# Kernel optimization log

Measured on AMD Instinct MI355X. Metric: run time of the kernel, lower is better.

The kernel has to match this reference:

```python
import jax, jax.numpy as jnp
import numpy as np

H = 16        # num query heads
HKV = 1       # num key/value heads (MQA; source matmul broadcasts only for 1 or H)
D = 128       # head_dim
SCALE = 1.0 / np.sqrt(D)


def setup_inputs() -> dict:
    key = jax.random.key(0)
    k1, k2, k3 = jax.random.split(key, 3)
    B, S, HID = 2, 2048, 2048
    hidden_states = jax.random.normal(k1, (B, S, HID), dtype=jnp.float32)
    # real RoPE tables: cos/sin of shape [S, D]
    inv_freq = 1.0 / (10000.0 ** (np.arange(0, D, 2, dtype=np.float32) / D))
    t = np.arange(S, dtype=np.float32)
    freqs = np.outer(t, inv_freq)                      # [S, D/2]
    emb = np.concatenate([freqs, freqs], axis=-1)      # [S, D]
    cos = jnp.asarray(np.cos(emb), dtype=jnp.float32)
    sin = jnp.asarray(np.sin(emb), dtype=jnp.float32)
    w_qkv = jax.random.normal(k2, (HID, (H + 2 * HKV) * D), dtype=jnp.float32) * (HID ** -0.5)
    w_o = jax.random.normal(k3, (H * D, HID), dtype=jnp.float32) * ((H * D) ** -0.5)
    return {"hidden_states": hidden_states, "cos": cos, "sin": sin,
            "w_qkv": w_qkv, "w_o": w_o}


def _rotate_half(x):
    x1, x2 = jnp.split(x, 2, axis=-1)
    return jnp.concatenate([-x2, x1], axis=-1)


def reference(hidden_states, cos, sin, w_qkv, w_o):
    B, S, _ = hidden_states.shape
    qkv = hidden_states @ w_qkv                        # [B,S,(H+2*HKV)*D]
    qkv = qkv.reshape(B, S, H + 2 * HKV, D)
    q = qkv[:, :, :H]                                  # [B,S,H,D]
    k = qkv[:, :, H:H + HKV]                           # [B,S,HKV,D]
    v = qkv[:, :, H + HKV:]                            # [B,S,HKV,D]
    c = cos[None, :, None, :]                          # [1,S,1,D]
    s = sin[None, :, None, :]
    q = q * c + _rotate_half(q) * s
    k = k * c + _rotate_half(k) * s
    # MQA: squeeze the single kv head
    k0 = k[:, :, 0]                                    # [B,S,D]
    v0 = v[:, :, 0]                                    # [B,S,D]
    qh = jnp.transpose(q, (0, 2, 1, 3))                # [B,H,S,D]
    scores = jnp.einsum('bhsd,btd->bhst', qh, k0) * SCALE
    attn = jax.nn.softmax(scores.astype(jnp.float32), axis=-1).astype(qh.dtype)
    out = jnp.einsum('bhst,btd->bhsd', attn, v0)       # [B,H,S,D]
    out = jnp.transpose(out, (0, 2, 1, 3)).reshape(B, S, H * D)
    return out @ w_o
```

## Files before the change

kernel.cpp:

```cpp
#include <hip/hip_runtime.h>

typedef __attribute__((ext_vector_type(8))) short bf16x8;
typedef __attribute__((ext_vector_type(4))) float f32x4;
typedef __attribute__((ext_vector_type(8))) unsigned short u16x8;
typedef __attribute__((ext_vector_type(2))) unsigned int u32x2;

#define H_Q   16
#define NH    18
#define SEQ   2048
#define BATCH 2
#define HID   2048
#define NQKV  2304
#define QK_SCALE2 0.1275174313f

__device__ __forceinline__ float bf2f(unsigned short u){
  union { unsigned int u; float f; } x; x.u = ((unsigned int)u) << 16; return x.f;
}
__device__ __forceinline__ unsigned short f2bf(float f){
  union { float f; unsigned int u; } x; x.f = f;
  unsigned int r = x.u + 0x7fffu + ((x.u >> 16) & 1u);
  return (unsigned short)(r >> 16);
}
__device__ __forceinline__ unsigned int cvtpk(float lo, float hi){
  unsigned int r;
  asm("v_cvt_pk_bf16_f32 %0, %1, %2" : "=v"(r) : "v"(lo), "v"(hi));
  return r;
}

__global__ __launch_bounds__(256) void convert_bf16(const float* __restrict__ src,
                                                    unsigned short* __restrict__ dst){
  const size_t i0 = ((size_t)blockIdx.x * 256 + threadIdx.x) * 16;
  f32x4 a = *(const f32x4*)(src + i0);
  f32x4 b = *(const f32x4*)(src + i0 + 4);
  f32x4 c = *(const f32x4*)(src + i0 + 8);
  f32x4 d = *(const f32x4*)(src + i0 + 12);
  u16x8 lo, hi;
#pragma unroll
  for (int j = 0; j < 4; ++j){
    lo[j] = f2bf(a[j]); lo[4+j] = f2bf(b[j]);
    hi[j] = f2bf(c[j]); hi[4+j] = f2bf(d[j]);
  }
  *(u16x8*)(dst + i0)     = lo;
  *(u16x8*)(dst + i0 + 8) = hi;
}

__global__ __launch_bounds__(256) void transpose_f2b(const float* __restrict__ W,
                                                     unsigned short* __restrict__ WT,
                                                     int K, int N){
  __shared__ float tile[64][72];
  const int t = threadIdx.x;
  const int nt = blockIdx.x * 64, kt = blockIdx.y * 64;
#pragma unroll
  for (int p = 0; p < 2; ++p){
    int slot = p*256 + t, r = slot >> 3, c = (slot & 7) * 8;
    *(f32x4*)&tile[r][c]     = *(const f32x4*)(W + (size_t)(kt + r)*N + nt + c);
    *(f32x4*)&tile[r][c + 4] = *(const f32x4*)(W + (size_t)(kt + r)*N + nt + c + 4);
  }
  __syncthreads();
#pragma unroll
  for (int p = 0; p < 2; ++p){
    int slot = p*256 + t, r = slot >> 3, c = (slot & 7) * 8;
    u16x8 v;
#pragma unroll
    for (int j = 0; j < 8; ++j) v[j] = f2bf(tile[c + j][r]);
    *(u16x8*)(WT + (size_t)(nt + r)*K + kt + c) = v;
  }
}

template<bool F32OUT>
__global__ __launch_bounds__(256, 2) void gemm_bt(const unsigned short* __restrict__ A,
                                                  const unsigned short* __restrict__ Bt,
                                                  void* __restrict__ Cv,
                                                  int M, int N, int K){
  __shared__ unsigned short lds[2][2][128*32];
  const int tid  = threadIdx.x;
  const int wave = tid >> 6, lane = tid & 63;
  const int row0 = blockIdx.x * 128, col0 = blockIdx.y * 128;
  const int wr = (wave >> 1) * 64, wc = (wave & 1) * 64;
  const int lm = lane & 15, lk = (lane >> 4) * 8;
  f32x4 acc[4][4] = {};

  auto stage = [&](int buf, int kt){
#pragma unroll
    for (int i = 0; i < 2; ++i){
      int slot = i*256 + tid;
      int r = slot >> 2, kc = (slot & 3) * 8;
      const unsigned short* ga = A  + (size_t)(row0 + r)*K + kt*32 + kc;
      const unsigned short* gb = Bt + (size_t)(col0 + r)*K + kt*32 + kc;
      unsigned short* la = &lds[buf][0][(i*256 + (wave << 6)) * 8];
      unsigned short* lb = &lds[buf][1][(i*256 + (wave << 6)) * 8];
      __builtin_amdgcn_global_load_lds((const __attribute__((address_space(1))) void*)ga,
                                       (__attribute__((address_space(3))) void*)la, 16, 0, 0);
      __builtin_amdgcn_global_load_lds((const __attribute__((address_space(1))) void*)gb,
                                       (__attribute__((address_space(3))) void*)lb, 16, 0, 0);
    }
  };

  stage(0, 0);
  const int KT = K >> 5;
  int buf = 0;
  for (int kt = 0; kt < KT; ++kt){
    __syncthreads();
    if (kt + 1 < KT) stage(buf ^ 1, kt + 1);
    const unsigned short* la = lds[buf][0];
    const unsigned short* lb = lds[buf][1];
    bf16x8 af[4], bfr[4];
#pragma unroll
    for (int i = 0; i < 4; ++i) af[i]  = *(const bf16x8*)&la[(wr + i*16 + lm)*32 + lk];
#pragma unroll
    for (int j = 0; j < 4; ++j) bfr[j] = *(const bf16x8*)&lb[(wc + j*16 + lm)*32 + lk];
#pragma unroll
    for (int i = 0; i < 4; ++i)
#pragma unroll
      for (int j = 0; j < 4; ++j)
        acc[i][j] = __builtin_amdgcn_mfma_f32_16x16x32_bf16(af[i], bfr[j], acc[i][j], 0, 0, 0);
    buf ^= 1;
  }

#pragma unroll
  for (int i = 0; i < 4; ++i){
    int row = row0 + wr + i*16 + (lane >> 4) * 4;
#pragma unroll
    for (int j = 0; j < 4; ++j){
      int col = col0 + wc + j*16 + lm;
#pragma unroll
      for (int r = 0; r < 4; ++r){
        if (F32OUT) ((float*)Cv)[(size_t)(row + r)*N + col] = acc[i][j][r];
        else ((unsigned short*)Cv)[(size_t)(row + r)*N + col] = f2bf(acc[i][j][r]);
      }
    }
  }
}

__global__ __launch_bounds__(256) void rope_pack(unsigned short* __restrict__ qkv,
                                                 const float* __restrict__ cosb,
                                                 const float* __restrict__ sinb,
                                                 unsigned short* __restrict__ Kb,
                                                 unsigned short* __restrict__ Vt){
  const int bs = blockIdx.x;
  const int s = bs & (SEQ-1), b = bs >> 11;
  const int t = threadIdx.x;
  unsigned short* row = qkv + (size_t)bs * NQKV;
  const float* cr = cosb + (size_t)s * 128;
  const float* sr = sinb + (size_t)s * 128;
  const int h = t >> 4, d0 = (t & 15) * 4;
  unsigned short* q = row + h * 128;
#pragma unroll
  for (int i = 0; i < 4; ++i){
    int d = d0 + i;
    float c  = cr[d], sn = sr[d];
    float x1 = bf2f(q[d]),  x2 = bf2f(q[d + 64]);
    q[d]      = f2bf((x1*c - x2*sn) * QK_SCALE2);
    q[d + 64] = f2bf((x2*c + x1*sn) * QK_SCALE2);
  }
  if (t < 64){
    const unsigned short* kk = row + H_Q*128;
    int d = t;
    float c  = cr[d], sn = sr[d];
    float x1 = bf2f(kk[d]), x2 = bf2f(kk[d + 64]);
    unsigned short* ko = Kb + ((size_t)b*SEQ + s)*128;
    ko[d]      = f2bf(x1*c - x2*sn);
    ko[d + 64] = f2bf(x2*c + x1*sn);
  }
  if (t < 128){
    Vt[((size_t)b*128 + t)*SEQ + s] = row[(H_Q + 1)*128 + t];
  }
}

__global__ __launch_bounds__(256, 2) void attn_fwd(const unsigned short* __restrict__ qkv,
                                                   const unsigned short* __restrict__ Kb,
                                                   const unsigned short* __restrict__ Vt,
                                                   unsigned short* __restrict__ Ob){
  __shared__ unsigned short kls[2][32*128];
  __shared__ unsigned short vls[2][128*32];
  const int tid = threadIdx.x, lane = tid & 63;
  const int g = lane >> 4, m = lane & 15;
  const int wg = blockIdx.x;
  const int bh = wg >> 4, qb = wg & 15;
  const int b = bh >> 4, h = bh & 15;
  const int q0 = qb * 128 + (tid >> 6) * 32;

  const unsigned short* qrowA = qkv + ((size_t)((b << 11) + q0 + m)*NH + h)*128;
  const unsigned short* qrowB = qrowA + (size_t)16*NH*128;
  bf16x8 qfA[4], qfB[4];
#pragma unroll
  for (int dc = 0; dc < 4; ++dc){
    qfA[dc] = *(const bf16x8*)(qrowA + dc*32 + g*8);
    qfB[dc] = *(const bf16x8*)(qrowB + dc*32 + g*8);
  }

  const unsigned short* Kbase = Kb + (size_t)b*SEQ*128;
  const unsigned short* Vbase = Vt + (size_t)b*128*SEQ;

  const int krow = tid >> 4;
  const int kchunk = (tid & 15) ^ (krow & 7);
  const int vrow = tid >> 2;
  const int vchunk = (tid & 3) ^ ((tid >> 3) & 3);

  auto stage = [&](int buf, int tile){
    const int n0 = tile * 32;
#pragma unroll
    for (int ck = 0; ck < 2; ++ck){
      const unsigned short* gp = Kbase + (size_t)(n0 + ck*16 + krow)*128 + kchunk*8;
      unsigned short* lp = &kls[buf][(ck*256 + tid) * 8];
      __builtin_amdgcn_global_load_lds((const __attribute__((address_space(1))) void*)gp,
                                       (__attribute__((address_space(3))) void*)lp, 16, 0, 0);
    }
#pragma unroll
    for (int cv = 0; cv < 2; ++cv){
      const unsigned short* gp = Vbase + (size_t)(cv*64 + vrow)*SEQ + n0 + vchunk*8;
      unsigned short* lp = &vls[buf][(cv*256 + tid) * 8];
      __builtin_amdgcn_global_load_lds((const __attribute__((address_space(1))) void*)gp,
                                       (__attribute__((address_space(3))) void*)lp, 16, 0, 0);
    }
  };

  f32x4 oA[8] = {}, oB[8] = {};
  float sA = 0.f, sB = 0.f;
  const int ksw = (m & 7);
  const int vsw = (m >> 1) & 3;

  stage(0, 0);
  stage(1, 1);
  const int NT = SEQ / 32;
  for (int t = 0; t < NT; ++t){
    const int cur = t & 1;
    if (t + 1 < NT) asm volatile("s_waitcnt vmcnt(4)" ::: "memory");
    else            asm volatile("s_waitcnt vmcnt(0)" ::: "memory");
    __builtin_amdgcn_s_barrier();

    const unsigned short* kb = kls[cur];
    const unsigned short* vb = vls[cur];

    bf16x8 kf[8];
#pragma unroll
    for (int dc = 0; dc < 4; ++dc){
      kf[dc]     = *(const bf16x8*)&kb[(size_t)m*128 + ((dc*4 + g) ^ ksw)*8];
      kf[4 + dc] = *(const bf16x8*)&kb[(size_t)(16 + m)*128 + ((dc*4 + g) ^ ksw)*8];
    }

    f32x4 a0 = {0,0,0,0}, a1 = {0,0,0,0}, c0 = {0,0,0,0}, c1 = {0,0,0,0};
    __builtin_amdgcn_s_setprio(1);
#pragma unroll
    for (int dc = 0; dc < 4; ++dc){
      a0 = __builtin_amdgcn_mfma_f32_16x16x32_bf16(kf[dc], qfA[dc], a0, 0, 0, 0);
      c0 = __builtin_amdgcn_mfma_f32_16x16x32_bf16(kf[dc], qfB[dc], c0, 0, 0, 0);
    }
#pragma unroll
    for (int dc = 0; dc < 4; ++dc){
      a1 = __builtin_amdgcn_mfma_f32_16x16x32_bf16(kf[4 + dc], qfA[dc], a1, 0, 0, 0);
      c1 = __builtin_amdgcn_mfma_f32_16x16x32_bf16(kf[4 + dc], qfB[dc], c1, 0, 0, 0);
    }
    __builtin_amdgcn_s_setprio(0);

    bf16x8 vf[8];
#pragma unroll
    for (int dt = 0; dt < 8; ++dt)
      vf[dt] = *(const bf16x8*)&vb[(size_t)(dt*16 + m)*32 + ((g ^ vsw))*8];

    asm volatile("s_waitcnt lgkmcnt(0)" ::: "memory");
    __builtin_amdgcn_s_barrier();
    if (t + 2 < NT) stage(cur, t + 2);

    float pA0[4], pA1[4], pB0[4], pB1[4];
#pragma unroll
    for (int r = 0; r < 4; ++r){
      pA0[r] = exp2f(fminf(a0[r], 100.f)); sA += pA0[r];
      pA1[r] = exp2f(fminf(a1[r], 100.f)); sA += pA1[r];
      pB0[r] = exp2f(fminf(c0[r], 100.f)); sB += pB0[r];
      pB1[r] = exp2f(fminf(c1[r], 100.f)); sB += pB1[r];
    }

    unsigned int A01 = cvtpk(pA0[0], pA0[1]), A23 = cvtpk(pA0[2], pA0[3]);
    unsigned int A45 = cvtpk(pA1[0], pA1[1]), A67 = cvtpk(pA1[2], pA1[3]);
    u32x2 tA0 = __builtin_amdgcn_permlane32_swap(A01, A45, false, false);
    u32x2 wA02 = __builtin_amdgcn_permlane16_swap(tA0[0], tA0[1], false, false);
    u32x2 tA1 = __builtin_amdgcn_permlane32_swap(A23, A67, false, false);
    u32x2 wA13 = __builtin_amdgcn_permlane16_swap(tA1[0], tA1[1], false, false);
    union { unsigned int w[4]; bf16x8 v; } UA;
    UA.w[0] = wA02[0]; UA.w[1] = wA13[0]; UA.w[2] = wA02[1]; UA.w[3] = wA13[1];
    bf16x8 pfA = UA.v;

    unsigned int B01 = cvtpk(pB0[0], pB0[1]), B23 = cvtpk(pB0[2], pB0[3]);
    unsigned int B45 = cvtpk(pB1[0], pB1[1]), B67 = cvtpk(pB1[2], pB1[3]);
    u32x2 tB0 = __builtin_amdgcn_permlane32_swap(B01, B45, false, false);
    u32x2 wB02 = __builtin_amdgcn_permlane16_swap(tB0[0], tB0[1], false, false);
    u32x2 tB1 = __builtin_amdgcn_permlane32_swap(B23, B67, false, false);
    u32x2 wB13 = __builtin_amdgcn_permlane16_swap(tB1[0], tB1[1], false, false);
    union { unsigned int w[4]; bf16x8 v; } UB;
    UB.w[0] = wB02[0]; UB.w[1] = wB13[0]; UB.w[2] = wB02[1]; UB.w[3] = wB13[1];
    bf16x8 pfB = UB.v;

    __builtin_amdgcn_s_setprio(1);
#pragma unroll
    for (int dt = 0; dt < 8; ++dt){
      oA[dt] = __builtin_amdgcn_mfma_f32_16x16x32_bf16(pfA, vf[dt], oA[dt], 0, 0, 0);
      oB[dt] = __builtin_amdgcn_mfma_f32_16x16x32_bf16(pfB, vf[dt], oB[dt], 0, 0, 0);
    }
    __builtin_amdgcn_s_setprio(0);
  }

  sA += __shfl_xor(sA, 16); sA += __shfl_xor(sA, 32);
  sB += __shfl_xor(sB, 16); sB += __shfl_xor(sB, 32);
  float invA = 1.f / sA, invB = 1.f / sB;
  float ivA[4], ivB[4];
#pragma unroll
  for (int r = 0; r < 4; ++r){
    ivA[r] = __shfl(invA, g*4 + r);
    ivB[r] = __shfl(invB, g*4 + r);
  }
  unsigned short* orowA = Ob + (size_t)((b << 11) + q0)*HID + h*128;
  unsigned short* orowB = orowA + (size_t)16*HID;
#pragma unroll
  for (int dt = 0; dt < 8; ++dt)
#pragma unroll
    for (int r = 0; r < 4; ++r){
      orowA[(size_t)(g*4 + r)*HID + dt*16 + m] = f2bf(oA[dt][r] * ivA[r]);
      orowB[(size_t)(g*4 + r)*HID + dt*16 + m] = f2bf(oB[dt][r] * ivB[r]);
    }
}

extern "C" void kernel_launch(void* const* d_in, const int* in_sizes, int n_in,
                              void* d_out, int out_size, void* d_ws, size_t ws_size,
                              hipStream_t stream){
  const float* hidden = (const float*)d_in[0];
  const float* cosb   = (const float*)d_in[1];
  const float* sinb   = (const float*)d_in[2];
  const float* wqkv   = (const float*)d_in[3];
  const float* wo     = (const float*)d_in[4];
  float* out = (float*)d_out;

  char* ws = (char*)d_ws;
  unsigned short* qkvb  = (unsigned short*)ws; ws += (size_t)BATCH*SEQ*NQKV*2;
  unsigned short* hidb  = (unsigned short*)ws; ws += (size_t)BATCH*SEQ*HID*2;
  unsigned short* attnb = hidb;
  unsigned short* Kbf   = (unsigned short*)ws; ws += (size_t)BATCH*SEQ*128*2;
  unsigned short* Vt    = (unsigned short*)ws; ws += (size_t)BATCH*SEQ*128*2;
  unsigned short* wqkvT = (unsigned short*)ws; ws += (size_t)NQKV*HID*2;
  unsigned short* woT   = wqkvT;

  convert_bf16<<<dim3(BATCH*SEQ*HID/4096), 256, 0, stream>>>(hidden, hidb);
  transpose_f2b<<<dim3(NQKV/64, HID/64), 256, 0, stream>>>(wqkv, wqkvT, HID, NQKV);
  gemm_bt<false><<<dim3(BATCH*SEQ/128, NQKV/128), 256, 0, stream>>>(hidb, wqkvT, qkvb,
                                                                    BATCH*SEQ, NQKV, HID);
  rope_pack<<<dim3(BATCH*SEQ), 256, 0, stream>>>(qkvb, cosb, sinb, Kbf, Vt);
  transpose_f2b<<<dim3(HID/64, HID/64), 256, 0, stream>>>(wo, woT, HID, HID);
  attn_fwd<<<dim3(SEQ/128 * BATCH*H_Q), 256, 0, stream>>>(qkvb, Kbf, Vt, attnb);
  gemm_bt<true><<<dim3(BATCH*SEQ/128, HID/128), 256, 0, stream>>>(attnb, woT, out,
                                                                  BATCH*SEQ, HID, HID);
}
```

Before: 209.9 us.

## Double attention KV tile to 64 keys per stage and use native exp2

The attention loop now stages 64 keys of K and V per buffer instead of 32. This halves the number of barrier and wait rounds, and each iteration processes two 32-key subtiles through a shared softmax/PV lambda. The V LDS layout and swizzle are changed to 64-wide rows. The exp2f call is replaced with the amdgcn exp2 builtin when available, to avoid the library's range handling. LDS usage doubles, which may reduce occupancy, and register pressure rises.

After: 198.0 us, median of 2. 5.6% less time.

```diff
diff --git a/kernel.cpp b/kernel.cpp
--- a/kernel.cpp
+++ b/kernel.cpp
@@ -12,6 +12,15 @@
 #define HID   2048
 #define NQKV  2304
 #define QK_SCALE2 0.1275174313f
+
+#if defined(__has_builtin)
+# if __has_builtin(__builtin_amdgcn_exp2f)
+#  define EXP2(x) __builtin_amdgcn_exp2f(x)
+# endif
+#endif
+#ifndef EXP2
+# define EXP2(x) exp2f(x)
+#endif
 
 __device__ __forceinline__ float bf2f(unsigned short u){
   union { unsigned int u; float f; } x; x.u = ((unsigned int)u) << 16; return x.f;
@@ -171,8 +180,8 @@
                                                    const unsigned short* __restrict__ Kb,
                                                    const unsigned short* __restrict__ Vt,
                                                    unsigned short* __restrict__ Ob){
-  __shared__ unsigned short kls[2][32*128];
-  __shared__ unsigned short vls[2][128*32];
+  __shared__ unsigned short kls[2][64*128];
+  __shared__ unsigned short vls[2][128*64];
   const int tid = threadIdx.x, lane = tid & 63;
   const int g = lane >> 4, m = lane & 15;
   const int wg = blockIdx.x;
@@ -194,21 +203,21 @@
 
   const int krow = tid >> 4;
   const int kchunk = (tid & 15) ^ (krow & 7);
-  const int vrow = tid >> 2;
-  const int vchunk = (tid & 3) ^ ((tid >> 3) & 3);
+  const int vrow = tid >> 3;
+  const int vchunk = (tid & 7) ^ (vrow & 7);
 
   auto stage = [&](int buf, int tile){
-    const int n0 = tile * 32;
-#pragma unroll
-    for (int ck = 0; ck < 2; ++ck){
+    const int n0 = tile * 64;
+#pragma unroll
+    for (int ck = 0; ck < 4; ++ck){
       const unsigned short* gp = Kbase + (size_t)(n0 + ck*16 + krow)*128 + kchunk*8;
       unsigned short* lp = &kls[buf][(ck*256 + tid) * 8];
       __builtin_amdgcn_global_load_lds((const __attribute__((address_space(1))) void*)gp,
                                        (__attribute__((address_space(3))) void*)lp, 16, 0, 0);
     }
 #pragma unroll
-    for (int cv = 0; cv < 2; ++cv){
-      const unsigned short* gp = Vbase + (size_t)(cv*64 + vrow)*SEQ + n0 + vchunk*8;
+    for (int cv = 0; cv < 4; ++cv){
+      const unsigned short* gp = Vbase + (size_t)(cv*32 + vrow)*SEQ + n0 + vchunk*8;
       unsigned short* lp = &vls[buf][(cv*256 + tid) * 8];
       __builtin_amdgcn_global_load_lds((const __attribute__((address_space(1))) void*)gp,
                                        (__attribute__((address_space(3))) void*)lp, 16, 0, 0);
@@ -218,59 +227,17 @@
   f32x4 oA[8] = {}, oB[8] = {};
   float sA = 0.f, sB = 0.f;
   const int ksw = (m & 7);
-  const int vsw = (m >> 1) & 3;
-
-  stage(0, 0);
-  stage(1, 1);
-  const int NT = SEQ / 32;
-  for (int t = 0; t < NT; ++t){
-    const int cur = t & 1;
-    if (t + 1 < NT) asm volatile("s_waitcnt vmcnt(4)" ::: "memory");
-    else            asm volatile("s_waitcnt vmcnt(0)" ::: "memory");
-    __builtin_amdgcn_s_barrier();
-
-    const unsigned short* kb = kls[cur];
-    const unsigned short* vb = vls[cur];
-
-    bf16x8 kf[8];
-#pragma unroll
-    for (int dc = 0; dc < 4; ++dc){
-      kf[dc]     = *(const bf16x8*)&kb[(size_t)m*128 + ((dc*4 + g) ^ ksw)*8];
-      kf[4 + dc] = *(const bf16x8*)&kb[(size_t)(16 + m)*128 + ((dc*4 + g) ^ ksw)*8];
-    }
-
-    f32x4 a0 = {0,0,0,0}, a1 = {0,0,0,0}, c0 = {0,0,0,0}, c1 = {0,0,0,0};
-    __builtin_amdgcn_s_setprio(1);
-#pragma unroll
-    for (int dc = 0; dc < 4; ++dc){
-      a0 = __builtin_amdgcn_mfma_f32_16x16x32_bf16(kf[dc], qfA[dc], a0, 0, 0, 0);
-      c0 = __builtin_amdgcn_mfma_f32_16x16x32_bf16(kf[dc], qfB[dc], c0, 0, 0, 0);
-    }
-#pragma unroll
-    for (int dc = 0; dc < 4; ++dc){
-      a1 = __builtin_amdgcn_mfma_f32_16x16x32_bf16(kf[4 + dc], qfA[dc], a1, 0, 0, 0);
-      c1 = __builtin_amdgcn_mfma_f32_16x16x32_bf16(kf[4 + dc], qfB[dc], c1, 0, 0, 0);
-    }
-    __builtin_amdgcn_s_setprio(0);
-
-    bf16x8 vf[8];
-#pragma unroll
-    for (int dt = 0; dt < 8; ++dt)
-      vf[dt] = *(const bf16x8*)&vb[(size_t)(dt*16 + m)*32 + ((g ^ vsw))*8];
-
-    asm volatile("s_waitcnt lgkmcnt(0)" ::: "memory");
-    __builtin_amdgcn_s_barrier();
-    if (t + 2 < NT) stage(cur, t + 2);
-
+  const int vsw = (m & 7);
+
+  auto process = [&](f32x4 a0, f32x4 a1, f32x4 c0, f32x4 c1, const bf16x8* vf){
     float pA0[4], pA1[4], pB0[4], pB1[4];
 #pragma unroll
     for (int r = 0; r < 4; ++r){
-      pA0[r] = exp2f(fminf(a0[r], 100.f)); sA += pA0[r];
-      pA1[r] = exp2f(fminf(a1[r], 100.f)); sA += pA1[r];
-      pB0[r] = exp2f(fminf(c0[r], 100.f)); sB += pB0[r];
-      pB1[r] = exp2f(fminf(c1[r], 100.f)); sB += pB1[r];
-    }
-
+      pA0[r] = EXP2(fminf(a0[r], 100.f)); sA += pA0[r];
+      pA1[r] = EXP2(fminf(a1[r], 100.f)); sA += pA1[r];
+      pB0[r] = EXP2(fminf(c0[r], 100.f)); sB += pB0[r];
+      pB1[r] = EXP2(fminf(c1[r], 100.f)); sB += pB1[r];
+    }
     unsigned int A01 = cvtpk(pA0[0], pA0[1]), A23 = cvtpk(pA0[2], pA0[3]);
     unsigned int A45 = cvtpk(pA1[0], pA1[1]), A67 = cvtpk(pA1[2], pA1[3]);
     u32x2 tA0 = __builtin_amdgcn_permlane32_swap(A01, A45, false, false);
@@ -279,8 +246,6 @@
     u32x2 wA13 = __builtin_amdgcn_permlane16_swap(tA1[0], tA1[1], false, false);
     union { unsigned int w[4]; bf16x8 v; } UA;
     UA.w[0] = wA02[0]; UA.w[1] = wA13[0]; UA.w[2] = wA02[1]; UA.w[3] = wA13[1];
-    bf16x8 pfA = UA.v;
-
     unsigned int B01 = cvtpk(pB0[0], pB0[1]), B23 = cvtpk(pB0[2], pB0[3]);
     unsigned int B45 = cvtpk(pB1[0], pB1[1]), B67 = cvtpk(pB1[2], pB1[3]);
     u32x2 tB0 = __builtin_amdgcn_permlane32_swap(B01, B45, false, false);
@@ -289,15 +254,78 @@
     u32x2 wB13 = __builtin_amdgcn_permlane16_swap(tB1[0], tB1[1], false, false);
     union { unsigned int w[4]; bf16x8 v; } UB;
     UB.w[0] = wB02[0]; UB.w[1] = wB13[0]; UB.w[2] = wB02[1]; UB.w[3] = wB13[1];
-    bf16x8 pfB = UB.v;
-
     __builtin_amdgcn_s_setprio(1);
 #pragma unroll
     for (int dt = 0; dt < 8; ++dt){
-      oA[dt] = __builtin_amdgcn_mfma_f32_16x16x32_bf16(pfA, vf[dt], oA[dt], 0, 0, 0);
-      oB[dt] = __builtin_amdgcn_mfma_f32_16x16x32_bf16(pfB, vf[dt], oB[dt], 0, 0, 0);
+      oA[dt] = __builtin_amdgcn_mfma_f32_16x16x32_bf16(UA.v, vf[dt], oA[dt], 0, 0, 0);
+      oB[dt] = __builtin_amdgcn_mfma_f32_16x16x32_bf16(UB.v, vf[dt], oB[dt], 0, 0, 0);
     }
     __builtin_amdgcn_s_setprio(0);
+  };
+
+  stage(0, 0);
+  stage(1, 1);
+  const int NT = SEQ / 64;
+  for (int t = 0; t < NT; ++t){
+    const int cur = t & 1;
+    if (t + 1 < NT) asm volatile("s_waitcnt vmcnt(8)" ::: "memory");
+    else            asm volatile("s_waitcnt vmcnt(0)" ::: "memory");
+    __builtin_amdgcn_s_barrier();
+
+    const unsigned short* kb = kls[cur];
+    const unsigned short* vb = vls[cur];
+
+    bf16x8 kf[8], vf[8];
+#pragma unroll
+    for (int dc = 0; dc < 4; ++dc){
+      kf[dc]     = *(const bf16x8*)&kb[(size_t)m*128 + ((dc*4 + g) ^ ksw)*8];
+      kf[4 + dc] = *(const bf16x8*)&kb[(size_t)(16 + m)*128 + ((dc*4 + g) ^ ksw)*8];
+    }
+    f32x4 a0 = {0,0,0,0}, a1 = {0,0,0,0}, c0 = {0,0,0,0}, c1 = {0,0,0,0};
+    __builtin_amdgcn_s_setprio(1);
+#pragma unroll
+    for (int dc = 0; dc < 4; ++dc){
+      a0 = __builtin_amdgcn_mfma_f32_16x16x32_bf16(kf[dc], qfA[dc], a0, 0, 0, 0);
+      c0 = __builtin_amdgcn_mfma_f32_16x16x32_bf16(kf[dc], qfB[dc], c0, 0, 0, 0);
+    }
+#pragma unroll
+    for (int dc = 0; dc < 4; ++dc){
+      a1 = __builtin_amdgcn_mfma_f32_16x16x32_bf16(kf[4 + dc], qfA[dc], a1, 0, 0, 0);
+      c1 = __builtin_amdgcn_mfma_f32_16x16x32_bf16(kf[4 + dc], qfB[dc], c1, 0, 0, 0);
+    }
+    __builtin_amdgcn_s_setprio(0);
+#pragma unroll
+    for (int dt = 0; dt < 8; ++dt)
+      vf[dt] = *(const bf16x8*)&vb[(size_t)(dt*16 + m)*64 + ((g ^ vsw))*8];
+    process(a0, a1, c0, c1, vf);
+
+#pragma unroll
+    for (int dc = 0; dc < 4; ++dc){
+      kf[dc]     = *(const bf16x8*)&kb[(size_t)(32 + m)*128 + ((dc*4 + g) ^ ksw)*8];
+      kf[4 + dc] = *(const bf16x8*)&kb[(size_t)(48 + m)*128 + ((dc*4 + g) ^ ksw)*8];
+    }
+    f32x4 a2 = {0,0,0,0}, a3 = {0,0,0,0}, c2 = {0,0,0,0}, c3 = {0,0,0,0};
+    __builtin_amdgcn_s_setprio(1);
+#pragma unroll
+    for (int dc = 0; dc < 4; ++dc){
+      a2 = __builtin_amdgcn_mfma_f32_16x16x32_bf16(kf[dc], qfA[dc], a2, 0, 0, 0);
+      c2 = __builtin_amdgcn_mfma_f32_16x16x32_bf16(kf[dc], qfB[dc], c2, 0, 0, 0);
+    }
+#pragma unroll
+    for (int dc = 0; dc < 4; ++dc){
+      a3 = __builtin_amdgcn_mfma_f32_16x16x32_bf16(kf[4 + dc], qfA[dc], a3, 0, 0, 0);
+      c3 = __builtin_amdgcn_mfma_f32_16x16x32_bf16(kf[4 + dc], qfB[dc], c3, 0, 0, 0);
+    }
+    __builtin_amdgcn_s_setprio(0);
+#pragma unroll
+    for (int dt = 0; dt < 8; ++dt)
+      vf[dt] = *(const bf16x8*)&vb[(size_t)(dt*16 + m)*64 + (((4 + g) ^ vsw))*8];
+
+    asm volatile("s_waitcnt lgkmcnt(0)" ::: "memory");
+    __builtin_amdgcn_s_barrier();
+    if (t + 2 < NT) stage(cur, t + 2);
+
+    process(a2, a3, c2, c3, vf);
   }
 
   sA += __shfl_xor(sA, 16); sA += __shfl_xor(sA, 32);
```
